# Performance work log

Hardware: AMD Instinct MI355X
Metric: run time of the kernel (lower is better)

The kernel has to match this reference:

```python
import jax, jax.numpy as jnp
import numpy as np

N, H, E, ATTR = 50000, 256, 800000, 107


def _ln(x, g, b, eps=1e-5):
    mu = jnp.mean(x, axis=-1, keepdims=True)
    v = jnp.mean((x - mu) ** 2, axis=-1, keepdims=True)
    return (x - mu) * jax.lax.rsqrt(v + eps) * g + b


def _gcn(x, src, dst, ew, W, b, n):
    # PyG GCNConv with edge_weight: add self-loops (weight 1), symmetric norm
    loop = jnp.arange(n)
    src = jnp.concatenate([src, loop])
    dst = jnp.concatenate([dst, loop])
    ew = jnp.concatenate([ew, jnp.ones((n,), ew.dtype)])
    deg = jax.ops.segment_sum(ew, dst, num_segments=n)  # [n]
    dinv = jnp.where(deg > 0, jax.lax.rsqrt(deg), 0.0)
    norm = dinv[src] * ew * dinv[dst]  # [E+n]
    h = x @ W.T  # [n,H] linear transform first
    agg = jax.ops.segment_sum(norm[:, None] * h[src], dst, num_segments=n)
    return agg + b


def setup_inputs() -> dict:
    key = jax.random.key(0)
    ks = jax.random.split(key, 12)
    s = 1.0 / np.sqrt(H)
    return {
        "x_struct": jax.random.normal(ks[0], (N, H), jnp.float32),
        "edge_index_bold": jax.random.randint(ks[1], (2, E), 0, N),
        "edge_attr_bold": jax.random.uniform(ks[2], (E,), jnp.float32),  # positive weights
        "edge_index_temp": jax.random.randint(ks[3], (2, E), 0, N),
        "edge_attr_temp": jax.random.uniform(ks[4], (E, ATTR), jnp.float32),
        "Wb": jax.random.normal(ks[5], (H, H), jnp.float32) * s,
        "bb": jnp.zeros((H,), jnp.float32),
        "Wt": jax.random.normal(ks[6], (H, H), jnp.float32) * s,
        "bt": jnp.zeros((H,), jnp.float32),
        "W1": jax.random.normal(ks[7], (H, ATTR), jnp.float32) * (1.0 / np.sqrt(ATTR)),
        "b1": jnp.zeros((H,), jnp.float32),
        "g1": jnp.ones((H,), jnp.float32),
        "be1": jnp.zeros((H,), jnp.float32),
        "W2": jax.random.normal(ks[8], (1, H), jnp.float32) * 0.01,
        "b2": jnp.ones((1,), jnp.float32),  # keep temporal edge weights positive
        "gs": jnp.ones((H,), jnp.float32),
        "bs": jnp.zeros((H,), jnp.float32),
        "gt": jnp.ones((H,), jnp.float32),
        "btn": jnp.zeros((H,), jnp.float32),
    }


def reference(x_struct, edge_attr_bold, edge_attr_temp, Wb, bb, Wt, bt,
              W1, b1, g1, be1, W2, b2, gs, bs, gt, btn,
              edge_index_bold, edge_index_temp):
    x = x_struct
    orig = x
    # BOLD-correlation GCN stage: gcn -> residual -> LN -> ReLU
    out = _gcn(x, edge_index_bold[0], edge_index_bold[1], edge_attr_bold, Wb, bb, N)
    x = jax.nn.relu(_ln(out + x, gs, bs))
    # temporal edge-weight MLP: Linear(107->H) -> LN -> ReLU -> Linear(H->1) -> squeeze
    h = jax.nn.relu(_ln(edge_attr_temp @ W1.T + b1, g1, be1))
    w = (h @ W2.T + b2)[:, 0]  # [E]
    # temporal GCN stage: gcn -> residual -> LN -> ReLU
    out = _gcn(x, edge_index_temp[0], edge_index_temp[1], w, Wt, bt, N)
    x = jax.nn.relu(_ln(out + x, gt, btn))
    # final residual with original input through struct_norm
    return _ln(x + orig, gs, bs)
```

## Files before the change

kernel.cpp:

```cpp
#include <hip/hip_runtime.h>

#define HDIM 256
#define KA 107
#define KAP 128

typedef short bf16x8 __attribute__((ext_vector_type(8)));
typedef float f32x4 __attribute__((ext_vector_type(4)));
typedef unsigned short ushort_t;

__device__ inline unsigned short f2bf(float f) {
    union { float f; unsigned u; } v; v.f = f;
    unsigned r = v.u + 0x7fff + ((v.u >> 16) & 1);
    return (unsigned short)(r >> 16);
}

__device__ inline unsigned cvt_pk_bf16(float a, float b) {
    unsigned r;
    asm("v_cvt_pk_bf16_f32 %0, %1, %2" : "=v"(r) : "v"(a), "v"(b));
    return r;
}

__device__ inline float bf_lo(unsigned u) { union { unsigned v; float f; } x; x.v = u << 16; return x.f; }
__device__ inline float bf_hi(unsigned u) { union { unsigned v; float f; } x; x.v = u & 0xffff0000u; return x.f; }

__device__ inline float4 guarded_load4(const float* p, size_t off, size_t tot) {
    if (off + 4 <= tot) return *(const float4*)(p + off);
    float4 r = {0.f, 0.f, 0.f, 0.f};
    float* rr = (float*)&r;
    for (int e = 0; e < 4; ++e) if (off + e < tot) rr[e] = p[off + e];
    return r;
}


__global__ void init_kernel(float* deg, int* cnt, int n) {
    int i = blockIdx.x * 256 + threadIdx.x;
    if (i < n) { deg[i] = 1.0f; cnt[i] = 0; }
}

__global__ void hist_kernel(const int* __restrict__ dst, const float* __restrict__ w,
                            float* deg, int* cnt, int ne) {
    int e = blockIdx.x * 256 + threadIdx.x;
    if (e < ne) {
        int d = dst[e];
        atomicAdd(&deg[d], w[e]);
        atomicAdd(&cnt[d], 1);
    }
}

__global__ void f32_to_bf16_kernel(const float* __restrict__ in, ushort_t* __restrict__ out, int n4) {
    int i = blockIdx.x * 256 + threadIdx.x;
    if (i < n4) {
        float4 v = ((const float4*)in)[i];
        uint2 o;
        o.x = cvt_pk_bf16(v.x, v.y);
        o.y = cvt_pk_bf16(v.z, v.w);
        ((uint2*)out)[i] = o;
    }
}

__global__ __launch_bounds__(256) void scan_a_kernel(const int* __restrict__ cnt,
                                                     float* deg, int* __restrict__ bsum, int n) {
    const int tid = threadIdx.x;
    const int i = blockIdx.x * 256 + tid;
    int v = (i < n) ? cnt[i] : 0;
    if (i < n) { float d = deg[i]; deg[i] = d > 0.f ? rsqrtf(d) : 0.f; }
    int s = v;
#pragma unroll
    for (int d = 1; d < 64; d <<= 1) s += __shfl_xor(s, d);
    __shared__ int ws[4];
    if ((tid & 63) == 0) ws[tid >> 6] = s;
    __syncthreads();
    if (tid == 0) bsum[blockIdx.x] = ws[0] + ws[1] + ws[2] + ws[3];
}

__global__ __launch_bounds__(256) void scan_b_kernel(int* __restrict__ bsum, int nb) {
    const int tid = threadIdx.x;
    int v = (tid < nb) ? bsum[tid] : 0;
    const int lane = tid & 63, wid = tid >> 6;
    int incl = v;
#pragma unroll
    for (int d = 1; d < 64; d <<= 1) { int m = __shfl_up(incl, d); if (lane >= d) incl += m; }
    __shared__ int ws[4];
    if (lane == 63) ws[wid] = incl;
    __syncthreads();
    if (tid < 4) {
        int wv = ws[tid];
        int iv = wv;
#pragma unroll
        for (int d = 1; d < 4; d <<= 1) { int m = __shfl_up(iv, d, 4); if (tid >= d) iv += m; }
        ws[tid] = iv - wv;
    }
    __syncthreads();
    if (tid < nb) bsum[tid] = (incl - v) + ws[wid];
}

__global__ __launch_bounds__(256) void scan_c_kernel(const int* __restrict__ cnt,
                                                     const int* __restrict__ bsum,
                                                     int* __restrict__ rptr,
                                                     int* __restrict__ cur, int n) {
    const int tid = threadIdx.x;
    const int i = blockIdx.x * 256 + tid;
    int v = (i < n) ? cnt[i] : 0;
    const int lane = tid & 63, wid = tid >> 6;
    int incl = v;
#pragma unroll
    for (int d = 1; d < 64; d <<= 1) { int m = __shfl_up(incl, d); if (lane >= d) incl += m; }
    __shared__ int ws[4];
    if (lane == 63) ws[wid] = incl;
    __syncthreads();
    if (tid < 4) {
        int wv = ws[tid];
        int iv = wv;
#pragma unroll
        for (int d = 1; d < 4; d <<= 1) { int m = __shfl_up(iv, d, 4); if (tid >= d) iv += m; }
        ws[tid] = iv - wv;
    }
    __syncthreads();
    const int excl = (incl - v) + ws[wid] + bsum[blockIdx.x];
    if (i < n) { rptr[i] = excl; cur[i] = excl; }
    if (i == n - 1) rptr[n] = excl + v;
}

__global__ void fill_kernel(const int* __restrict__ src, const int* __restrict__ dst,
                            const float* __restrict__ w, const float* __restrict__ dinv,
                            int* cur, uint2* __restrict__ edata, int ne) {
    int e = blockIdx.x * 256 + threadIdx.x;
    if (e < ne) {
        int s = src[e], d = dst[e];
        int pos = atomicAdd(&cur[d], 1);
        uint2 ed;
        ed.x = (unsigned)s;
        ed.y = __float_as_uint(dinv[s] * w[e] * dinv[d]);
        edata[pos] = ed;
    }
}

__global__ __launch_bounds__(256) void agg_kernel(const ushort_t* __restrict__ Xb,
                                                  const int* __restrict__ rptr,
                                                  const uint2* __restrict__ edata,
                                                  const float* __restrict__ dinv,
                                                  ushort_t* __restrict__ out, int n) {
    const int v = blockIdx.x * 4 + (threadIdx.x >> 6);
    if (v >= n) return;
    const int lane = threadIdx.x & 63;
    const float dv = dinv[v];
    const uint2 xv = *(const uint2*)(Xb + (size_t)v * HDIM + lane * 4);
    const float dv2 = dv * dv;
    float a0[8], a1[8], a2[8], a3[8];
#pragma unroll
    for (int c = 0; c < 8; ++c) { a0[c] = 0.f; a1[c] = 0.f; a2[c] = 0.f; a3[c] = 0.f; }
    a0[0] = dv2 * bf_lo(xv.x); a1[0] = dv2 * bf_hi(xv.x);
    a2[0] = dv2 * bf_lo(xv.y); a3[0] = dv2 * bf_hi(xv.y);

    const int b = rptr[v];
    const int total = rptr[v + 1] - b;
    uint2 pv[16]; float pn[16];
#pragma unroll
    for (int c = 0; c < 16; ++c) {
        if (c < total) {
            uint2 ed = edata[b + c];
            pn[c] = __uint_as_float(ed.y);
            pv[c] = *(const uint2*)(Xb + (size_t)ed.x * HDIM + lane * 4);
        }
    }
    for (int base = 0; base < total; base += 16) {
#pragma unroll
        for (int c = 0; c < 16; ++c) {
            if (base + c < total) {
                uint2 cv = pv[c]; float cn = pn[c];
                int nx = base + 16 + c;
                if (nx < total) {
                    uint2 ed = edata[b + nx];
                    pn[c] = __uint_as_float(ed.y);
                    pv[c] = *(const uint2*)(Xb + (size_t)ed.x * HDIM + lane * 4);
                }
                const int s8 = c & 7;
                a0[s8] = fmaf(cn, bf_lo(cv.x), a0[s8]);
                a1[s8] = fmaf(cn, bf_hi(cv.x), a1[s8]);
                a2[s8] = fmaf(cn, bf_lo(cv.y), a2[s8]);
                a3[s8] = fmaf(cn, bf_hi(cv.y), a3[s8]);
            }
        }
    }
    float r0 = ((a0[0] + a0[1]) + (a0[2] + a0[3])) + ((a0[4] + a0[5]) + (a0[6] + a0[7]));
    float r1 = ((a1[0] + a1[1]) + (a1[2] + a1[3])) + ((a1[4] + a1[5]) + (a1[6] + a1[7]));
    float r2 = ((a2[0] + a2[1]) + (a2[2] + a2[3])) + ((a2[4] + a2[5]) + (a2[6] + a2[7]));
    float r3 = ((a3[0] + a3[1]) + (a3[2] + a3[3])) + ((a3[4] + a3[5]) + (a3[6] + a3[7]));
    uint2 o;
    o.x = cvt_pk_bf16(r0, r1);
    o.y = cvt_pk_bf16(r2, r3);
    *(uint2*)(out + (size_t)v * HDIM + lane * 4) = o;
}

__global__ void prep_w_kernel(const float* __restrict__ W, ushort_t* __restrict__ Wp,
                              int K, int KP) {
    int i = blockIdx.x * 256 + threadIdx.x;
    if (i < 256 * KP) {
        int n = i / KP, k = i - n * KP;
        Wp[i] = (k < K) ? f2bf(W[n * K + k]) : (ushort_t)0;
    }
}

__global__ __launch_bounds__(256) void mlp_mfma_kernel(
    const float* __restrict__ A,
    const ushort_t* __restrict__ Wp,
    const float* __restrict__ b1v, const float* __restrict__ g1v,
    const float* __restrict__ be1v, const float* __restrict__ W2,
    const float* __restrict__ b2s, float* __restrict__ out,
    int M, int ntiles) {
    __shared__ ushort_t As[2][64][136];
    __shared__ float ps1[64][4], ps2[64][4], pd[64][4];
    const int tid = threadIdx.x;
    const int l = tid & 63, wv = tid >> 6, g = l >> 4, c = l & 15;
    const float b2sc = b2s[0];
    const size_t tot = (size_t)M * KA;

    for (int z = tid; z < 2 * 64 * 16; z += 256) {
        int buf = z >> 10;
        int rem = z & 1023;
        As[buf][rem >> 4][112 + (rem & 15)] = 0;
    }

    bf16x8 wreg[4][4];
    {
        const ushort_t* wb = Wp + (size_t)(wv * 64 + c) * KAP + g * 8;
#pragma unroll
        for (int ks = 0; ks < 4; ++ks)
#pragma unroll
            for (int nt = 0; nt < 4; ++nt)
                wreg[ks][nt] = *(const bf16x8*)(wb + nt * 16 * KAP + ks * 32);
    }

    const int srow = tid >> 2, sj = tid & 3;
    float4 sreg[7];

    const int t0 = blockIdx.x;
    if (t0 < ntiles) {
        const size_t roff = (size_t)(t0 * 64 + srow) * KA + sj * 4;
#pragma unroll
        for (int i = 0; i < 7; ++i) sreg[i] = guarded_load4(A, roff + i * 16, tot);
#pragma unroll
        for (int i = 0; i < 7; ++i) {
            uint2 o;
            o.x = cvt_pk_bf16(sreg[i].x, sreg[i].y);
            o.y = cvt_pk_bf16(sreg[i].z, sreg[i].w);
            *(uint2*)&As[0][srow][sj * 4 + i * 16] = o;
        }
    }
    __syncthreads();

    int cur = 0;
    for (int t = t0; t < ntiles; t += gridDim.x) {
        const int tn = t + gridDim.x;
        const bool have_next = tn < ntiles;
        if (have_next) {
            const size_t roff = (size_t)(tn * 64 + srow) * KA + sj * 4;
#pragma unroll
            for (int i = 0; i < 7; ++i) sreg[i] = guarded_load4(A, roff + i * 16, tot);
        }

        f32x4 acc[4][4];
#pragma unroll
        for (int rt = 0; rt < 4; ++rt)
#pragma unroll
            for (int nt = 0; nt < 4; ++nt) acc[rt][nt] = (f32x4){0.f, 0.f, 0.f, 0.f};
        __builtin_amdgcn_s_setprio(1);
#pragma unroll
        for (int ks = 0; ks < 4; ++ks) {
            bf16x8 af[4];
#pragma unroll
            for (int rt = 0; rt < 4; ++rt)
                af[rt] = *(const bf16x8*)&As[cur][rt * 16 + c][ks * 32 + g * 8];
#pragma unroll
            for (int nt = 0; nt < 4; ++nt)
#pragma unroll
                for (int rt = 0; rt < 4; ++rt)
                    acc[rt][nt] = __builtin_amdgcn_mfma_f32_16x16x32_bf16(wreg[ks][nt], af[rt], acc[rt][nt], 0, 0, 0);
        }
        __builtin_amdgcn_s_setprio(0);

        const int nb = wv * 64 + (g << 2);
        const int m0 = t * 64;
#pragma unroll
        for (int rt = 0; rt < 4; ++rt) {
            float s1 = 0.f, s2 = 0.f;
#pragma unroll
            for (int nt = 0; nt < 4; ++nt) {
                const float4 b4 = *(const float4*)(b1v + nb + nt * 16);
                f32x4 v = acc[rt][nt];
                v[0] += b4.x; v[1] += b4.y; v[2] += b4.z; v[3] += b4.w;
                acc[rt][nt] = v;
                s1 += v[0] + v[1] + v[2] + v[3];
                s2 += v[0] * v[0] + v[1] * v[1] + v[2] * v[2] + v[3] * v[3];
            }
            s1 += __shfl_xor(s1, 16); s1 += __shfl_xor(s1, 32);
            s2 += __shfl_xor(s2, 16); s2 += __shfl_xor(s2, 32);
            if (l < 16) { ps1[rt * 16 + c][wv] = s1; ps2[rt * 16 + c][wv] = s2; }
        }
        __syncthreads();
#pragma unroll
        for (int rt = 0; rt < 4; ++rt) {
            float4 p1 = *(const float4*)ps1[rt * 16 + c];
            float4 p2 = *(const float4*)ps2[rt * 16 + c];
            float s1 = p1.x + p1.y + p1.z + p1.w;
            float s2 = p2.x + p2.y + p2.z + p2.w;
            float mu = s1 * (1.f / HDIM);
            float var = s2 * (1.f / HDIM) - mu * mu;
            float rs = rsqrtf(var + 1e-5f);
            float dacc = 0.f;
#pragma unroll
            for (int nt = 0; nt < 4; ++nt) {
                const float4 g4 = *(const float4*)(g1v + nb + nt * 16);
                const float4 e4 = *(const float4*)(be1v + nb + nt * 16);
                const float4 w4 = *(const float4*)(W2 + nb + nt * 16);
                f32x4 v = acc[rt][nt];
                float y0 = fmaxf((v[0] - mu) * rs * g4.x + e4.x, 0.f);
                float y1 = fmaxf((v[1] - mu) * rs * g4.y + e4.y, 0.f);
                float y2 = fmaxf((v[2] - mu) * rs * g4.z + e4.z, 0.f);
                float y3 = fmaxf((v[3] - mu) * rs * g4.w + e4.w, 0.f);
                dacc = fmaf(y0, w4.x, dacc); dacc = fmaf(y1, w4.y, dacc);
                dacc = fmaf(y2, w4.z, dacc); dacc = fmaf(y3, w4.w, dacc);
            }
            dacc += __shfl_xor(dacc, 16); dacc += __shfl_xor(dacc, 32);
            if (l < 16) pd[rt * 16 + c][wv] = dacc;
        }
        if (have_next) {
#pragma unroll
            for (int i = 0; i < 7; ++i) {
                uint2 o;
                o.x = cvt_pk_bf16(sreg[i].x, sreg[i].y);
                o.y = cvt_pk_bf16(sreg[i].z, sreg[i].w);
                *(uint2*)&As[cur ^ 1][srow][sj * 4 + i * 16] = o;
            }
        }
        __syncthreads();
        if (tid < 64) {
            float4 p = *(const float4*)pd[tid];
            int gr = m0 + tid;
            if (gr < M) out[gr] = p.x + p.y + p.z + p.w + b2sc;
        }
        cur ^= 1;
    }
}

template <int MODE>
__global__ __launch_bounds__(256) void gemm_node_kernel(
    const ushort_t* __restrict__ A,
    const ushort_t* __restrict__ Wp,
    const float* __restrict__ bias,
    const ushort_t* __restrict__ res_bf,
    const ushort_t* __restrict__ orig_bf,
    const float* __restrict__ g1v, const float* __restrict__ b1v,
    const float* __restrict__ g2v, const float* __restrict__ b2v,
    float* __restrict__ out, ushort_t* __restrict__ out_bf, int M) {
    __shared__ ushort_t As[64][264];
    __shared__ float ps1[64][4], ps2[64][4], ps3[64][4], ps4[64][4];
    const int tid = threadIdx.x;
    const int m0 = blockIdx.x * 64;
    const int l = tid & 63, wv = tid >> 6, g = l >> 4, c = l & 15;

    {
        const int r = tid >> 2, j = tid & 3;
        const ushort_t* gsrc = A + (size_t)(m0 + r) * HDIM;
        const bool ok = (m0 + r) < M;
#pragma unroll
        for (int i = 0; i < 8; ++i) {
            const int ci = i * 4 + j;
            bf16x8 v = (bf16x8){0,0,0,0,0,0,0,0};
            if (ok) v = *(const bf16x8*)(gsrc + ci * 8);
            *(bf16x8*)&As[r][ci * 8] = v;
        }
    }
    __syncthreads();

    f32x4 acc[4][4];
#pragma unroll
    for (int rt = 0; rt < 4; ++rt)
#pragma unroll
        for (int nt = 0; nt < 4; ++nt) acc[rt][nt] = (f32x4){0.f, 0.f, 0.f, 0.f};

    const ushort_t* wb = Wp + (size_t)(wv * 64 + c) * HDIM + g * 8;
    __builtin_amdgcn_s_setprio(1);
#pragma unroll
    for (int ks = 0; ks < 8; ++ks) {
        bf16x8 af[4];
#pragma unroll
        for (int rt = 0; rt < 4; ++rt)
            af[rt] = *(const bf16x8*)&As[rt * 16 + c][ks * 32 + g * 8];
#pragma unroll
        for (int nt = 0; nt < 4; ++nt) {
            bf16x8 bfr = *(const bf16x8*)(wb + nt * 16 * HDIM + ks * 32);
#pragma unroll
            for (int rt = 0; rt < 4; ++rt)
                acc[rt][nt] = __builtin_amdgcn_mfma_f32_16x16x32_bf16(bfr, af[rt], acc[rt][nt], 0, 0, 0);
        }
    }
    __builtin_amdgcn_s_setprio(0);

    const int nb = wv * 64 + (g << 2);
#pragma unroll
    for (int rt = 0; rt < 4; ++rt) {
        const int m = m0 + rt * 16 + c;
        const bool vm = m < M;
        const ushort_t* rrow = res_bf + (size_t)m * HDIM + nb;
        float s1 = 0.f, s2 = 0.f;
#pragma unroll
        for (int nt = 0; nt < 4; ++nt) {
            const float4 b4 = *(const float4*)(bias + nb + nt * 16);
            float4 r4 = {0.f, 0.f, 0.f, 0.f};
            if (vm) {
                uint2 rb = *(const uint2*)(rrow + nt * 16);
                r4.x = bf_lo(rb.x); r4.y = bf_hi(rb.x);
                r4.z = bf_lo(rb.y); r4.w = bf_hi(rb.y);
            }
            f32x4 v = acc[rt][nt];
            v[0] += b4.x + r4.x; v[1] += b4.y + r4.y;
            v[2] += b4.z + r4.z; v[3] += b4.w + r4.w;
            acc[rt][nt] = v;
            s1 += v[0] + v[1] + v[2] + v[3];
            s2 += v[0] * v[0] + v[1] * v[1] + v[2] * v[2] + v[3] * v[3];
        }
        s1 += __shfl_xor(s1, 16); s1 += __shfl_xor(s1, 32);
        s2 += __shfl_xor(s2, 16); s2 += __shfl_xor(s2, 32);
        if (l < 16) { ps1[rt * 16 + c][wv] = s1; ps2[rt * 16 + c][wv] = s2; }
    }
    __syncthreads();
#pragma unroll
    for (int rt = 0; rt < 4; ++rt) {
        const int m = m0 + rt * 16 + c;
        const bool vm = m < M;
        float4 p1 = *(const float4*)ps1[rt * 16 + c];
        float4 p2 = *(const float4*)ps2[rt * 16 + c];
        float s1 = p1.x + p1.y + p1.z + p1.w;
        float s2 = p2.x + p2.y + p2.z + p2.w;
        float mu = s1 * (1.f / HDIM);
        float var = s2 * (1.f / HDIM) - mu * mu;
        float rs = rsqrtf(var + 1e-5f);
        if constexpr (MODE == 0) {
            ushort_t* obrow = out_bf + (size_t)m * HDIM + nb;
#pragma unroll
            for (int nt = 0; nt < 4; ++nt) {
                const float4 g4 = *(const float4*)(g1v + nb + nt * 16);
                const float4 e4 = *(const float4*)(b1v + nb + nt * 16);
                f32x4 v = acc[rt][nt];
                float o0 = fmaxf((v[0] - mu) * rs * g4.x + e4.x, 0.f);
                float o1 = fmaxf((v[1] - mu) * rs * g4.y + e4.y, 0.f);
                float o2 = fmaxf((v[2] - mu) * rs * g4.z + e4.z, 0.f);
                float o3 = fmaxf((v[3] - mu) * rs * g4.w + e4.w, 0.f);
                if (vm) {
                    uint2 ob;
                    ob.x = cvt_pk_bf16(o0, o1);
                    ob.y = cvt_pk_bf16(o2, o3);
                    *(uint2*)(obrow + nt * 16) = ob;
                }
            }
        } else {
            const ushort_t* grow = orig_bf + (size_t)m * HDIM + nb;
            float t1 = 0.f, t2 = 0.f;
#pragma unroll
            for (int nt = 0; nt < 4; ++nt) {
                const float4 g4 = *(const float4*)(g1v + nb + nt * 16);
                const float4 e4 = *(const float4*)(b1v + nb + nt * 16);
                float4 o4 = {0.f, 0.f, 0.f, 0.f};
                if (vm) {
                    uint2 gb = *(const uint2*)(grow + nt * 16);
                    o4.x = bf_lo(gb.x); o4.y = bf_hi(gb.x);
                    o4.z = bf_lo(gb.y); o4.w = bf_hi(gb.y);
                }
                f32x4 v = acc[rt][nt];
                f32x4 u;
                u[0] = fmaxf((v[0] - mu) * rs * g4.x + e4.x, 0.f) + o4.x;
                u[1] = fmaxf((v[1] - mu) * rs * g4.y + e4.y, 0.f) + o4.y;
                u[2] = fmaxf((v[2] - mu) * rs * g4.z + e4.z, 0.f) + o4.z;
                u[3] = fmaxf((v[3] - mu) * rs * g4.w + e4.w, 0.f) + o4.w;
                acc[rt][nt] = u;
                t1 += u[0] + u[1] + u[2] + u[3];
                t2 += u[0] * u[0] + u[1] * u[1] + u[2] * u[2] + u[3] * u[3];
            }
            t1 += __shfl_xor(t1, 16); t1 += __shfl_xor(t1, 32);
            t2 += __shfl_xor(t2, 16); t2 += __shfl_xor(t2, 32);
            if (l < 16) { ps3[rt * 16 + c][wv] = t1; ps4[rt * 16 + c][wv] = t2; }
        }
    }
    if constexpr (MODE == 1) {
        __syncthreads();
#pragma unroll
        for (int rt = 0; rt < 4; ++rt) {
            const int m = m0 + rt * 16 + c;
            const bool vm = m < M;
            float4 p1 = *(const float4*)ps3[rt * 16 + c];
            float4 p2 = *(const float4*)ps4[rt * 16 + c];
            float s1 = p1.x + p1.y + p1.z + p1.w;
            float s2 = p2.x + p2.y + p2.z + p2.w;
            float mu2 = s1 * (1.f / HDIM);
            float var2 = s2 * (1.f / HDIM) - mu2 * mu2;
            float rs2 = rsqrtf(var2 + 1e-5f);
            float* orow = out + (size_t)m * HDIM + nb;
#pragma unroll
            for (int nt = 0; nt < 4; ++nt) {
                const float4 g4 = *(const float4*)(g2v + nb + nt * 16);
                const float4 e4 = *(const float4*)(b2v + nb + nt * 16);
                f32x4 u = acc[rt][nt];
                float4 o;
                o.x = (u[0] - mu2) * rs2 * g4.x + e4.x;
                o.y = (u[1] - mu2) * rs2 * g4.y + e4.y;
                o.z = (u[2] - mu2) * rs2 * g4.z + e4.z;
                o.w = (u[3] - mu2) * rs2 * g4.w + e4.w;
                if (vm) *(float4*)(orow + nt * 16) = o;
            }
        }
    }
}


extern "C" void kernel_launch(void* const* d_in, const int* in_sizes, int n_in,
                              void* d_out, int out_size, void* d_ws, size_t ws_size,
                              hipStream_t stream) {
    const float* x    = (const float*)d_in[0];
    const int*   eib  = (const int*)d_in[1];
    const float* eab  = (const float*)d_in[2];
    const int*   eit  = (const int*)d_in[3];
    const float* eat  = (const float*)d_in[4];
    const float* Wb   = (const float*)d_in[5];
    const float* bb   = (const float*)d_in[6];
    const float* Wt   = (const float*)d_in[7];
    const float* bt   = (const float*)d_in[8];
    const float* W1   = (const float*)d_in[9];
    const float* b1   = (const float*)d_in[10];
    const float* g1   = (const float*)d_in[11];
    const float* be1  = (const float*)d_in[12];
    const float* W2   = (const float*)d_in[13];
    const float* b2   = (const float*)d_in[14];
    const float* gs   = (const float*)d_in[15];
    const float* bs   = (const float*)d_in[16];
    const float* gt   = (const float*)d_in[17];
    const float* btn  = (const float*)d_in[18];

    const int Nn = in_sizes[0] / HDIM;
    const int Ne = in_sizes[2];

    const int* src_b = eib;  const int* dst_b = eib + Ne;
    const int* src_t = eit;  const int* dst_t = eit + Ne;

    char* w = (char*)d_ws;
    ushort_t* aggb = (ushort_t*)w; w += (size_t)Nn * HDIM * 2;
    ushort_t* xb   = (ushort_t*)w; w += (size_t)Nn * HDIM * 2;
    ushort_t* x1b  = (ushort_t*)w; w += (size_t)Nn * HDIM * 2;
    float*    wtmp = (float*)w;    w += (size_t)Ne * 4;
    float*    dinv = (float*)w;    w += (size_t)Nn * 4;
    int*      cnt  = (int*)w;      w += (size_t)Nn * 4;
    int*      rptr = (int*)w;      w += (size_t)(Nn + 4) * 4;
    int*      cur  = (int*)w;      w += (size_t)Nn * 4;
    uint2*    edata = (uint2*)w;   w += (size_t)Ne * 8;
    int*      bsum = (int*)w;      w += (size_t)256 * 4;
    ushort_t* W1p  = (ushort_t*)w; w += (size_t)256 * KAP * 2;
    ushort_t* Wbp  = (ushort_t*)w; w += (size_t)256 * 256 * 2;
    ushort_t* Wtp  = (ushort_t*)w; w += (size_t)256 * 256 * 2;

    float* out = (float*)d_out;
    dim3 b256(256);
    dim3 gN((Nn + 255) / 256), gE((Ne + 255) / 256);
    const int nbScan = (Nn + 255) / 256;
    dim3 gAgg((Nn + 3) / 4);
    dim3 gGemmN((Nn + 63) / 64);
    const int ntiles = (Ne + 63) / 64;
    dim3 gMlp(512);
    const int n4 = Nn * HDIM / 4;
    dim3 gCvt((n4 + 255) / 256);

    prep_w_kernel<<<dim3((256 * KAP + 255) / 256), b256, 0, stream>>>(W1, W1p, KA, KAP);
    prep_w_kernel<<<dim3((256 * 256 + 255) / 256), b256, 0, stream>>>(Wb, Wbp, 256, 256);
    prep_w_kernel<<<dim3((256 * 256 + 255) / 256), b256, 0, stream>>>(Wt, Wtp, 256, 256);
    f32_to_bf16_kernel<<<gCvt, b256, 0, stream>>>(x, xb, n4);

    init_kernel<<<gN, b256, 0, stream>>>(dinv, cnt, Nn);
    hist_kernel<<<gE, b256, 0, stream>>>(dst_b, eab, dinv, cnt, Ne);
    scan_a_kernel<<<dim3(nbScan), b256, 0, stream>>>(cnt, dinv, bsum, Nn);
    scan_b_kernel<<<dim3(1), b256, 0, stream>>>(bsum, nbScan);
    scan_c_kernel<<<dim3(nbScan), b256, 0, stream>>>(cnt, bsum, rptr, cur, Nn);
    fill_kernel<<<gE, b256, 0, stream>>>(src_b, dst_b, eab, dinv, cur, edata, Ne);
    agg_kernel<<<gAgg, b256, 0, stream>>>(xb, rptr, edata, dinv, aggb, Nn);
    gemm_node_kernel<0><<<gGemmN, b256, 0, stream>>>(
        aggb, Wbp, bb, xb, nullptr, gs, bs, nullptr, nullptr, nullptr, x1b, Nn);

    mlp_mfma_kernel<<<gMlp, b256, 0, stream>>>(
        eat, W1p, b1, g1, be1, W2, b2, wtmp, Ne, ntiles);

    init_kernel<<<gN, b256, 0, stream>>>(dinv, cnt, Nn);
    hist_kernel<<<gE, b256, 0, stream>>>(dst_t, wtmp, dinv, cnt, Ne);
    scan_a_kernel<<<dim3(nbScan), b256, 0, stream>>>(cnt, dinv, bsum, Nn);
    scan_b_kernel<<<dim3(1), b256, 0, stream>>>(bsum, nbScan);
    scan_c_kernel<<<dim3(nbScan), b256, 0, stream>>>(cnt, bsum, rptr, cur, Nn);
    fill_kernel<<<gE, b256, 0, stream>>>(src_t, dst_t, wtmp, dinv, cur, edata, Ne);
    agg_kernel<<<gAgg, b256, 0, stream>>>(x1b, rptr, edata, dinv, aggb, Nn);
    gemm_node_kernel<1><<<gGemmN, b256, 0, stream>>>(
        aggb, Wtp, bt, x1b, xb, gt, btn, gs, bs, out, nullptr, Nn);
}
```

Baseline: 821.0 us.

## Compute GCN degree from CSR segments instead of float atomics

```diff
diff --git a/kernel.cpp b/kernel.cpp
--- a/kernel.cpp
+++ b/kernel.cpp
@@ -32,19 +32,9 @@
 }
 
 
-__global__ void init_kernel(float* deg, int* cnt, int n) {
-    int i = blockIdx.x * 256 + threadIdx.x;
-    if (i < n) { deg[i] = 1.0f; cnt[i] = 0; }
-}
-
-__global__ void hist_kernel(const int* __restrict__ dst, const float* __restrict__ w,
-                            float* deg, int* cnt, int ne) {
+__global__ void hist_cnt_kernel(const int* __restrict__ dst, int* cnt, int ne) {
     int e = blockIdx.x * 256 + threadIdx.x;
-    if (e < ne) {
-        int d = dst[e];
-        atomicAdd(&deg[d], w[e]);
-        atomicAdd(&cnt[d], 1);
-    }
+    if (e < ne) atomicAdd(&cnt[dst[e]], 1);
 }
 
 __global__ void f32_to_bf16_kernel(const float* __restrict__ in, ushort_t* __restrict__ out, int n4) {
@@ -59,11 +49,10 @@
 }
 
 __global__ __launch_bounds__(256) void scan_a_kernel(const int* __restrict__ cnt,
-                                                     float* deg, int* __restrict__ bsum, int n) {
+                                                     int* __restrict__ bsum, int n) {
     const int tid = threadIdx.x;
     const int i = blockIdx.x * 256 + tid;
     int v = (i < n) ? cnt[i] : 0;
-    if (i < n) { float d = deg[i]; deg[i] = d > 0.f ? rsqrtf(d) : 0.f; }
     int s = v;
 #pragma unroll
     for (int d = 1; d < 64; d <<= 1) s += __shfl_xor(s, d);
@@ -122,16 +111,27 @@
 }
 
 __global__ void fill_kernel(const int* __restrict__ src, const int* __restrict__ dst,
-                            const float* __restrict__ w, const float* __restrict__ dinv,
+                            const float* __restrict__ w,
                             int* cur, uint2* __restrict__ edata, int ne) {
     int e = blockIdx.x * 256 + threadIdx.x;
     if (e < ne) {
-        int s = src[e], d = dst[e];
+        int d = dst[e];
         int pos = atomicAdd(&cur[d], 1);
         uint2 ed;
-        ed.x = (unsigned)s;
-        ed.y = __float_as_uint(dinv[s] * w[e] * dinv[d]);
+        ed.x = (unsigned)src[e];
+        ed.y = __float_as_uint(w[e]);
         edata[pos] = ed;
+    }
+}
+
+__global__ void deg_kernel(const uint2* __restrict__ edata, const int* __restrict__ rptr,
+                           float* __restrict__ dinv, int n) {
+    int v = blockIdx.x * 256 + threadIdx.x;
+    if (v < n) {
+        const int b = rptr[v], e = rptr[v + 1];
+        float s = 1.0f;
+        for (int i = b; i < e; ++i) s += __uint_as_float(edata[i].y);
+        dinv[v] = s > 0.f ? rsqrtf(s) : 0.f;
     }
 }
 
@@ -154,31 +154,30 @@
 
     const int b = rptr[v];
     const int total = rptr[v + 1] - b;
-    uint2 pv[16]; float pn[16];
-#pragma unroll
-    for (int c = 0; c < 16; ++c) {
+    uint2 pv[8]; float pn[8];
+#pragma unroll
+    for (int c = 0; c < 8; ++c) {
         if (c < total) {
             uint2 ed = edata[b + c];
-            pn[c] = __uint_as_float(ed.y);
+            pn[c] = dinv[ed.x] * __uint_as_float(ed.y) * dv;
             pv[c] = *(const uint2*)(Xb + (size_t)ed.x * HDIM + lane * 4);
         }
     }
-    for (int base = 0; base < total; base += 16) {
-#pragma unroll
-        for (int c = 0; c < 16; ++c) {
+    for (int base = 0; base < total; base += 8) {
+#pragma unroll
+        for (int c = 0; c < 8; ++c) {
             if (base + c < total) {
                 uint2 cv = pv[c]; float cn = pn[c];
-                int nx = base + 16 + c;
+                int nx = base + 8 + c;
                 if (nx < total) {
                     uint2 ed = edata[b + nx];
-                    pn[c] = __uint_as_float(ed.y);
+                    pn[c] = dinv[ed.x] * __uint_as_float(ed.y) * dv;
                     pv[c] = *(const uint2*)(Xb + (size_t)ed.x * HDIM + lane * 4);
                 }
-                const int s8 = c & 7;
-                a0[s8] = fmaf(cn, bf_lo(cv.x), a0[s8]);
-                a1[s8] = fmaf(cn, bf_hi(cv.x), a1[s8]);
-                a2[s8] = fmaf(cn, bf_lo(cv.y), a2[s8]);
-                a3[s8] = fmaf(cn, bf_hi(cv.y), a3[s8]);
+                a0[c] = fmaf(cn, bf_lo(cv.x), a0[c]);
+                a1[c] = fmaf(cn, bf_hi(cv.x), a1[c]);
+                a2[c] = fmaf(cn, bf_lo(cv.y), a2[c]);
+                a3[c] = fmaf(cn, bf_hi(cv.y), a3[c]);
             }
         }
     }
@@ -573,12 +572,13 @@
     prep_w_kernel<<<dim3((256 * 256 + 255) / 256), b256, 0, stream>>>(Wt, Wtp, 256, 256);
     f32_to_bf16_kernel<<<gCvt, b256, 0, stream>>>(x, xb, n4);
 
-    init_kernel<<<gN, b256, 0, stream>>>(dinv, cnt, Nn);
-    hist_kernel<<<gE, b256, 0, stream>>>(dst_b, eab, dinv, cnt, Ne);
-    scan_a_kernel<<<dim3(nbScan), b256, 0, stream>>>(cnt, dinv, bsum, Nn);
+    hipMemsetAsync(cnt, 0, (size_t)Nn * 4, stream);
+    hist_cnt_kernel<<<gE, b256, 0, stream>>>(dst_b, cnt, Ne);
+    scan_a_kernel<<<dim3(nbScan), b256, 0, stream>>>(cnt, bsum, Nn);
     scan_b_kernel<<<dim3(1), b256, 0, stream>>>(bsum, nbScan);
     scan_c_kernel<<<dim3(nbScan), b256, 0, stream>>>(cnt, bsum, rptr, cur, Nn);
-    fill_kernel<<<gE, b256, 0, stream>>>(src_b, dst_b, eab, dinv, cur, edata, Ne);
+    fill_kernel<<<gE, b256, 0, stream>>>(src_b, dst_b, eab, cur, edata, Ne);
+    deg_kernel<<<gN, b256, 0, stream>>>(edata, rptr, dinv, Nn);
     agg_kernel<<<gAgg, b256, 0, stream>>>(xb, rptr, edata, dinv, aggb, Nn);
     gemm_node_kernel<0><<<gGemmN, b256, 0, stream>>>(
         aggb, Wbp, bb, xb, nullptr, gs, bs, nullptr, nullptr, nullptr, x1b, Nn);
@@ -586,12 +586,13 @@
     mlp_mfma_kernel<<<gMlp, b256, 0, stream>>>(
         eat, W1p, b1, g1, be1, W2, b2, wtmp, Ne, ntiles);
 
-    init_kernel<<<gN, b256, 0, stream>>>(dinv, cnt, Nn);
-    hist_kernel<<<gE, b256, 0, stream>>>(dst_t, wtmp, dinv, cnt, Ne);
-    scan_a_kernel<<<dim3(nbScan), b256, 0, stream>>>(cnt, dinv, bsum, Nn);
+    hipMemsetAsync(cnt, 0, (size_t)Nn * 4, stream);
+    hist_cnt_kernel<<<gE, b256, 0, stream>>>(dst_t, cnt, Ne);
+    scan_a_kernel<<<dim3(nbScan), b256, 0, stream>>>(cnt, bsum, Nn);
     scan_b_kernel<<<dim3(1), b256, 0, stream>>>(bsum, nbScan);
     scan_c_kernel<<<dim3(nbScan), b256, 0, stream>>>(cnt, bsum, rptr, cur, Nn);
-    fill_kernel<<<gE, b256, 0, stream>>>(src_t, dst_t, wtmp, dinv, cur, edata, Ne);
+    fill_kernel<<<gE, b256, 0, stream>>>(src_t, dst_t, wtmp, cur, edata, Ne);
+    deg_kernel<<<gN, b256, 0, stream>>>(edata, rptr, dinv, Nn);
     agg_kernel<<<gAgg, b256, 0, stream>>>(x1b, rptr, edata, dinv, aggb, Nn);
     gemm_node_kernel<1><<<gGemmN, b256, 0, stream>>>(
         aggb, Wtp, bt, x1b, xb, gt, btn, gs, bs, out, nullptr, Nn);
```

Result: faster. 776.0 us (-5.5%).
